# Performance work log

Hardware: AMD Instinct MI355X
Metric: run time of the kernel (lower is better)

The kernel has to match this reference:

```python
import jax, jax.numpy as jnp
import numpy as np


def setup_inputs() -> dict:
    key = jax.random.key(0)
    ks = jax.random.split(key, 6)
    B, C, H, W = 4, 512, 64, 64
    C8 = C // 8
    NS = H * W  # broadcasting in the original forces num_styles == H*W
    x = jax.random.normal(ks[0], (B, C, H, W), dtype=jnp.float32)
    Wq = jax.random.normal(ks[1], (C8, C), dtype=jnp.float32) * 0.02
    bq = jnp.zeros((C8,), jnp.float32)
    Wk = jax.random.normal(ks[2], (C8, C), dtype=jnp.float32) * 0.02
    bk = jnp.zeros((C8,), jnp.float32)
    Wv = jax.random.normal(ks[3], (C, C), dtype=jnp.float32) * 0.02
    bv = jnp.zeros((C,), jnp.float32)
    gamma = jnp.full((1,), 0.5, jnp.float32)  # nonzero so attention path contributes
    style_idx = jax.random.randint(ks[4], (B,), 0, NS)
    return {"x": x, "Wq": Wq, "bq": bq, "Wk": Wk, "bk": bk,
            "Wv": Wv, "bv": bv, "gamma": gamma,
            "style_idx": style_idx, "num_styles": NS}


def reference(x, Wq, bq, Wk, bk, Wv, bv, gamma, style_idx, num_styles):
    B, C, H, W = x.shape
    N = H * W
    xf = x.reshape(B, C, N)                                   # [B,C,N]
    # 1x1 convs == per-pixel linear projections
    q = jnp.einsum('oc,bcn->bno', Wq, xf) + bq                # [B,N,C8]
    k = jnp.einsum('oc,bcn->bon', Wk, xf) + bk[None, :, None]  # [B,C8,N]
    v = jnp.einsum('oc,bcn->bon', Wv, xf) + bv[None, :, None]  # [B,C,N]
    attn = jax.nn.softmax(jnp.einsum('bno,bom->bnm', q, k), axis=2)  # [B,N,N]
    # style mask: num_styles everywhere, except [b, 0, style_idx[b]] = 0
    # (torch scatter_ with index shape [B,1,1] only touches row 0)
    sw = jnp.full((B, N, num_styles), jnp.asarray(num_styles, x.dtype))
    sw = sw.at[jnp.arange(B), 0, style_idx].set(0.0)
    attn = attn * sw
    attended = jnp.einsum('bcn,bmn->bcm', v, attn).reshape(B, C, H, W)
    return gamma * attended + x
```

## Files before the change

kernel.cpp:

```cpp
#include <hip/hip_runtime.h>

#define B_DIM 4
#define C_DIM 512
#define N_DIM 4096
#define NS_F 4096.0f

typedef __attribute__((ext_vector_type(8))) short bf16x8;
typedef __attribute__((ext_vector_type(4))) float f32x4;

__device__ __forceinline__ unsigned short f2bf(float f) {
    union { float f; unsigned int u; } a; a.f = f;
    unsigned int u = a.u;
    return (unsigned short)((u + 0x7fffu + ((u >> 16) & 1u)) >> 16);
}
__device__ __forceinline__ float bf2f(unsigned short s) {
    union { unsigned int u; float f; } a; a.u = ((unsigned int)s) << 16;
    return a.f;
}

__global__ __launch_bounds__(256) void wconv_kernel(
    const float* __restrict__ Wq, const float* __restrict__ Wk,
    const float* __restrict__ Wv, unsigned short* __restrict__ Wb)
{
    const int gid = blockIdx.x * 256 + threadIdx.x;
    const int flat = gid * 4;
    const float* src;
    if (flat < 32768)      src = Wq + flat;
    else if (flat < 65536) src = Wk + (flat - 32768);
    else                   src = Wv + (flat - 65536);
    float4 v = *(const float4*)src;
    ushort4 r;
    r.x = f2bf(v.x); r.y = f2bf(v.y); r.z = f2bf(v.z); r.w = f2bf(v.w);
    *(ushort4*)(Wb + flat) = r;
}

__global__ __launch_bounds__(256) void xt_kernel(
    const float* __restrict__ x, unsigned short* __restrict__ xT)
{
    const int b  = blockIdx.z;
    const int c0 = blockIdx.y * 64;
    const int n0 = blockIdx.x * 64;
    __shared__ float T[64][65];
    const int t   = threadIdx.x;
    const int l16 = t & 15;
    const int cr  = t >> 4;

    #pragma unroll
    for (int j = 0; j < 4; ++j) {
        const int c = cr + j * 16;
        float4 v = *(const float4*)(x + ((size_t)(b * C_DIM + c0 + c)) * N_DIM + n0 + l16 * 4);
        T[l16 * 4 + 0][c] = v.x;
        T[l16 * 4 + 1][c] = v.y;
        T[l16 * 4 + 2][c] = v.z;
        T[l16 * 4 + 3][c] = v.w;
    }
    __syncthreads();
    #pragma unroll
    for (int j = 0; j < 2; ++j) {
        const int chunk = t + j * 256;
        const int n  = chunk >> 3;
        const int c8 = (chunk & 7) * 8;
        bf16x8 r;
        #pragma unroll
        for (int e = 0; e < 8; ++e) r[e] = (short)f2bf(T[n][c8 + e]);
        *(bf16x8*)(xT + ((size_t)b * N_DIM + n0 + n) * 512 + c0 + c8) = r;
    }
}

__global__ __launch_bounds__(256, 4) void proj_kernel(
    const unsigned short* __restrict__ xT, const unsigned short* __restrict__ Wb,
    const float* __restrict__ bq, const float* __restrict__ bk,
    const float* __restrict__ bv,
    unsigned short* __restrict__ qB, unsigned short* __restrict__ kB,
    unsigned short* __restrict__ vB)
{
    const int ot = blockIdx.x;
    const int n0 = blockIdx.y * 64;
    const int b  = blockIdx.z;
    const int tid  = threadIdx.x;
    const int w    = tid >> 6;
    const int lane = tid & 63;
    const int lql  = lane & 15;
    const int lk4  = lane >> 4;

    f32x4 acc[4];
    #pragma unroll
    for (int og = 0; og < 4; ++og) acc[og] = (f32x4){0.f, 0.f, 0.f, 0.f};

    if (ot < 2) {
        const unsigned short* Wp = Wb + ot * 32768;
        const unsigned short* xa = xT + ((size_t)b * N_DIM + n0 + w * 16 + lql) * 512 + lk4 * 8;
        for (int c0 = 0; c0 < 512; c0 += 32) {
            bf16x8 a = *(const bf16x8*)(xa + c0);
            #pragma unroll
            for (int og = 0; og < 4; ++og) {
                bf16x8 wf = *(const bf16x8*)(Wp + (size_t)(og * 16 + lql) * 512 + c0 + lk4 * 8);
                acc[og] = __builtin_amdgcn_mfma_f32_16x16x32_bf16(a, wf, acc[og], 0, 0, 0);
            }
        }
        const float* bias = (ot == 0) ? bq : bk;
        #pragma unroll
        for (int og = 0; og < 4; ++og) {
            const float bb = bias[og * 16 + lql];
            #pragma unroll
            for (int r = 0; r < 4; ++r) {
                const int n = n0 + w * 16 + lk4 * 4 + r;
                const unsigned short val = f2bf(acc[og][r] + bb);
                if (ot == 0) {
                    qB[((size_t)b * N_DIM + n) * 64 + og * 16 + lql] = val;
                } else {
                    const int o = og * 16 + lql;
                    kB[((size_t)b * N_DIM + n) * 64 + (o ^ ((n & 7) << 3))] = val;
                }
            }
        }
    } else {
        const int cb0 = (ot - 2) * 64;
        const unsigned short* wa = Wb + 65536 + (size_t)(cb0 + w * 16 + lql) * 512 + lk4 * 8;
        const unsigned short* xb = xT + (size_t)b * N_DIM * 512;
        for (int c0 = 0; c0 < 512; c0 += 32) {
            bf16x8 a = *(const bf16x8*)(wa + c0);
            #pragma unroll
            for (int og = 0; og < 4; ++og) {
                bf16x8 xf = *(const bf16x8*)(xb + (size_t)(n0 + og * 16 + lql) * 512 + c0 + lk4 * 8);
                acc[og] = __builtin_amdgcn_mfma_f32_16x16x32_bf16(a, xf, acc[og], 0, 0, 0);
            }
        }
        #pragma unroll
        for (int r = 0; r < 4; ++r) {
            const int c = cb0 + w * 16 + lk4 * 4 + r;
            const float bb = bv[c];
            #pragma unroll
            for (int og = 0; og < 4; ++og) {
                vB[((size_t)(b * C_DIM + c)) * N_DIM + n0 + og * 16 + lql] =
                    f2bf(acc[og][r] + bb);
            }
        }
    }
}

__global__ __launch_bounds__(256, 4) void flash_kernel(
    const unsigned short* __restrict__ qB,
    const unsigned short* __restrict__ kB,
    const unsigned short* __restrict__ vB,
    const float* __restrict__ x,
    const float* __restrict__ gamma,
    float* __restrict__ stats,
    float* __restrict__ out)
{
    const int bid   = blockIdx.x;
    const int low3  = bid & 7;
    const int b     = low3 >> 1;
    const int c0bit = low3 & 1;
    const int high  = bid >> 3;
    const int mt    = high >> 1;
    const int ch    = ((high & 1) << 1) | c0bit;
    const int m0    = mt * 64;

    const int tid  = threadIdx.x;
    const int w    = tid >> 6;
    const int lane = tid & 63;
    const int lql  = lane & 15;
    const int lk4  = lane >> 4;
    const int swz  = (lql & 7) << 3;

    __shared__ __align__(16) unsigned short Kl[2][4096];
    __shared__ __align__(16) unsigned short Pl[4096];
    __shared__ float scl[64];
    __shared__ float ll[64];
    __shared__ int   fl[4];

    const unsigned short* qrow = qB + ((size_t)b * N_DIM + m0 + w * 16 + lql) * 64 + lk4 * 8;
    const bf16x8 qf0 = *(const bf16x8*)(qrow);
    const bf16x8 qf1 = *(const bf16x8*)(qrow + 32);

    f32x4 acc[2][4];
    #pragma unroll
    for (int cg = 0; cg < 2; ++cg)
        #pragma unroll
        for (int qg = 0; qg < 4; ++qg)
            acc[cg][qg] = (f32x4){0.f, 0.f, 0.f, 0.f};

    float m_run = -3.0e38f;
    float l_run = 0.f;

    const unsigned short* kbb = kB + (size_t)b * N_DIM * 64;
    const unsigned short* vbb = vB + (size_t)b * C_DIM * N_DIM;
    const int cs = ch * 128 + w * 32;

    {
        bf16x8 a0 = *(const bf16x8*)(kbb + tid * 16);
        bf16x8 a1 = *(const bf16x8*)(kbb + tid * 16 + 8);
        *(bf16x8*)(&Kl[0][tid * 16]) = a0;
        *(bf16x8*)(&Kl[0][tid * 16 + 8]) = a1;
    }
    __syncthreads();

    int buf = 0;
    for (int t = 0; t < 64; ++t) {
        const int tn_ = (t + 1) & 63;
        const bf16x8 kn0 = *(const bf16x8*)(kbb + (size_t)tn_ * 4096 + tid * 16);
        const bf16x8 kn1 = *(const bf16x8*)(kbb + (size_t)tn_ * 4096 + tid * 16 + 8);

        f32x4 s[4];
        #pragma unroll
        for (int g = 0; g < 4; ++g) {
            const unsigned short* kr = &Kl[buf][(g * 16 + lql) * 64];
            bf16x8 ka0 = *(const bf16x8*)(kr + ((lk4 * 8) ^ swz));
            bf16x8 ka1 = *(const bf16x8*)(kr + ((lk4 * 8 + 32) ^ swz));
            f32x4 z = (f32x4){0.f, 0.f, 0.f, 0.f};
            z = __builtin_amdgcn_mfma_f32_16x16x32_bf16(ka0, qf0, z, 0, 0, 0);
            z = __builtin_amdgcn_mfma_f32_16x16x32_bf16(ka1, qf1, z, 0, 0, 0);
            s[g] = z;
        }

        float pmax = s[0][0];
        #pragma unroll
        for (int g = 0; g < 4; ++g)
            #pragma unroll
            for (int r = 0; r < 4; ++r)
                pmax = fmaxf(pmax, s[g][r]);
        pmax = fmaxf(pmax, __shfl_xor(pmax, 16));
        pmax = fmaxf(pmax, __shfl_xor(pmax, 32));

        const int wflag = __any(pmax > m_run + 8.f);
        float scv = 1.f;
        if (wflag) {
            const float nm = fmaxf(m_run, pmax);
            scv = __expf(m_run - nm);
            m_run = nm;
        }
        float p[4][4];
        float ps = 0.f;
        #pragma unroll
        for (int g = 0; g < 4; ++g)
            #pragma unroll
            for (int r = 0; r < 4; ++r) {
                p[g][r] = __expf(s[g][r] - m_run);
                ps += p[g][r];
            }
        ps += __shfl_xor(ps, 16);
        ps += __shfl_xor(ps, 32);
        l_run = l_run * scv + ps;

        if (lk4 == 0) scl[w * 16 + lql] = scv;
        if (lane == 0) fl[w] = wflag;

        {
            const int prow = (w * 16 + lql) * 64;
            #pragma unroll
            for (int g = 0; g < 4; ++g) {
                unsigned int lo = (unsigned int)f2bf(p[g][0]) | ((unsigned int)f2bf(p[g][1]) << 16);
                unsigned int hi = (unsigned int)f2bf(p[g][2]) | ((unsigned int)f2bf(p[g][3]) << 16);
                *(uint2*)(&Pl[prow + ((g * 16 + lk4 * 4) ^ swz)]) = make_uint2(lo, hi);
            }
        }
        __syncthreads();

        *(bf16x8*)(&Kl[buf ^ 1][tid * 16]) = kn0;
        *(bf16x8*)(&Kl[buf ^ 1][tid * 16 + 8]) = kn1;

        const int bflag = fl[0] | fl[1] | fl[2] | fl[3];
        if (bflag) {
            float sc4[4];
            #pragma unroll
            for (int qg = 0; qg < 4; ++qg) sc4[qg] = scl[qg * 16 + lql];
            #pragma unroll
            for (int cg = 0; cg < 2; ++cg)
                #pragma unroll
                for (int qg = 0; qg < 4; ++qg) {
                    acc[cg][qg][0] *= sc4[qg];
                    acc[cg][qg][1] *= sc4[qg];
                    acc[cg][qg][2] *= sc4[qg];
                    acc[cg][qg][3] *= sc4[qg];
                }
        }

        bf16x8 pf[4][2];
        #pragma unroll
        for (int qg = 0; qg < 4; ++qg) {
            const unsigned short* pr = &Pl[(qg * 16 + lql) * 64];
            pf[qg][0] = *(const bf16x8*)(pr + ((lk4 * 8) ^ swz));
            pf[qg][1] = *(const bf16x8*)(pr + ((lk4 * 8 + 32) ^ swz));
        }

        const int n0 = t * 64;
        const unsigned short* vpb = vbb + (size_t)(cs + lql) * N_DIM + n0 + lk4 * 8;
        __builtin_amdgcn_s_setprio(1);
        #pragma unroll
        for (int cg = 0; cg < 2; ++cg) {
            const unsigned short* vp = vpb + (size_t)cg * 16 * N_DIM;
            bf16x8 va0 = *(const bf16x8*)(vp);
            bf16x8 va1 = *(const bf16x8*)(vp + 32);
            #pragma unroll
            for (int qg = 0; qg < 4; ++qg) {
                acc[cg][qg] = __builtin_amdgcn_mfma_f32_16x16x32_bf16(va0, pf[qg][0], acc[cg][qg], 0, 0, 0);
                acc[cg][qg] = __builtin_amdgcn_mfma_f32_16x16x32_bf16(va1, pf[qg][1], acc[cg][qg], 0, 0, 0);
            }
        }
        __builtin_amdgcn_s_setprio(0);
        __syncthreads();
        buf ^= 1;
    }

    if (mt == 0 && ch == 0 && tid == 0) {
        stats[b * 2 + 0] = m_run;
        stats[b * 2 + 1] = l_run;
    }

    if (lk4 == 0) ll[w * 16 + lql] = l_run;
    __syncthreads();

    const float gns = gamma[0] * NS_F;
    float inv4[4];
    #pragma unroll
    for (int qg = 0; qg < 4; ++qg) inv4[qg] = 1.f / ll[qg * 16 + lql];

    #pragma unroll
    for (int cg = 0; cg < 2; ++cg) {
        #pragma unroll
        for (int r = 0; r < 4; ++r) {
            const int c = cs + cg * 16 + lk4 * 4 + r;
            const size_t rowb = ((size_t)b * C_DIM + c) * N_DIM;
            #pragma unroll
            for (int qg = 0; qg < 4; ++qg) {
                const int mg = m0 + qg * 16 + lql;
                out[rowb + mg] = fmaf(gns * inv4[qg], acc[cg][qg][r], x[rowb + mg]);
            }
        }
    }
}

__global__ __launch_bounds__(512) void patch_kernel(
    const unsigned short* __restrict__ qB,
    const unsigned short* __restrict__ kB,
    const unsigned short* __restrict__ vB,
    const float* __restrict__ stats,
    const float* __restrict__ gamma,
    const int* __restrict__ sidx,
    float* __restrict__ out)
{
    const int b = blockIdx.x;
    const int c = threadIdx.x;
    __shared__ float q0s[64];
    if (c < 64) q0s[c] = bf2f(qB[(size_t)b * N_DIM * 64 + c]);
    __syncthreads();
    const int s  = sidx[b];
    const int m7 = s & 7;
    const unsigned short* kr = kB + ((size_t)b * N_DIM + s) * 64;
    float logit = 0.f;
    #pragma unroll
    for (int dj = 0; dj < 8; ++dj) {
        const int slot = dj ^ m7;
        bf16x8 kv = *(const bf16x8*)(kr + slot * 8);
        #pragma unroll
        for (int e = 0; e < 8; ++e)
            logit = fmaf(bf2f((unsigned short)kv[e]), q0s[dj * 8 + e], logit);
    }
    const float corr = NS_F * __expf(logit - stats[b * 2]) / stats[b * 2 + 1];
    const float g = gamma[0];
    const float vcs = bf2f(vB[((size_t)b * C_DIM + c) * N_DIM + s]);
    out[((size_t)b * C_DIM + c) * N_DIM] -= g * corr * vcs;
}

extern "C" void kernel_launch(void* const* d_in, const int* in_sizes, int n_in,
                              void* d_out, int out_size, void* d_ws, size_t ws_size,
                              hipStream_t stream)
{
    const float* x     = (const float*)d_in[0];
    const float* Wq    = (const float*)d_in[1];
    const float* bq    = (const float*)d_in[2];
    const float* Wk    = (const float*)d_in[3];
    const float* bk    = (const float*)d_in[4];
    const float* Wv    = (const float*)d_in[5];
    const float* bv    = (const float*)d_in[6];
    const float* gamma = (const float*)d_in[7];
    const int*   sidx  = (const int*)d_in[8];
    float* out = (float*)d_out;

    unsigned short* xT = (unsigned short*)d_ws;
    unsigned short* Wb = xT + (size_t)B_DIM * N_DIM * 512;
    unsigned short* qB = Wb + 327680;
    unsigned short* kB = qB + (size_t)B_DIM * N_DIM * 64;
    unsigned short* vB = kB + (size_t)B_DIM * N_DIM * 64;
    float* stats = (float*)(vB + (size_t)B_DIM * C_DIM * N_DIM);

    wconv_kernel<<<dim3(320), 256, 0, stream>>>(Wq, Wk, Wv, Wb);
    xt_kernel<<<dim3(64, 8, B_DIM), 256, 0, stream>>>(x, xT);
    proj_kernel<<<dim3(10, 64, B_DIM), 256, 0, stream>>>(xT, Wb, bq, bk, bv, qB, kB, vB);
    flash_kernel<<<dim3(1024), 256, 0, stream>>>(qB, kB, vB, x, gamma, stats, out);
    patch_kernel<<<dim3(B_DIM), 512, 0, stream>>>(qB, kB, vB, stats, gamma, sidx, out);
}
```

Before: 350.7 us.

## Fold log2e into Q, use exp2, padded P tile, hw bf16 pack, unrolled projections

```diff
diff --git a/kernel.cpp b/kernel.cpp
--- a/kernel.cpp
+++ b/kernel.cpp
@@ -4,6 +4,7 @@
 #define C_DIM 512
 #define N_DIM 4096
 #define NS_F 4096.0f
+#define LOG2E_F 1.4426950408889634f
 
 typedef __attribute__((ext_vector_type(8))) short bf16x8;
 typedef __attribute__((ext_vector_type(4))) float f32x4;
@@ -67,7 +68,7 @@
     }
 }
 
-__global__ __launch_bounds__(256, 4) void proj_kernel(
+__global__ __launch_bounds__(256, 2) void proj_kernel(
     const unsigned short* __restrict__ xT, const unsigned short* __restrict__ Wb,
     const float* __restrict__ bq, const float* __restrict__ bk,
     const float* __restrict__ bv,
@@ -90,12 +91,19 @@
     if (ot < 2) {
         const unsigned short* Wp = Wb + ot * 32768;
         const unsigned short* xa = xT + ((size_t)b * N_DIM + n0 + w * 16 + lql) * 512 + lk4 * 8;
-        for (int c0 = 0; c0 < 512; c0 += 32) {
-            bf16x8 a = *(const bf16x8*)(xa + c0);
-            #pragma unroll
-            for (int og = 0; og < 4; ++og) {
-                bf16x8 wf = *(const bf16x8*)(Wp + (size_t)(og * 16 + lql) * 512 + c0 + lk4 * 8);
-                acc[og] = __builtin_amdgcn_mfma_f32_16x16x32_bf16(a, wf, acc[og], 0, 0, 0);
+        #pragma unroll
+        for (int h = 0; h < 2; ++h) {
+            bf16x8 af[8];
+            #pragma unroll
+            for (int i = 0; i < 8; ++i)
+                af[i] = *(const bf16x8*)(xa + (h * 8 + i) * 32);
+            #pragma unroll
+            for (int i = 0; i < 8; ++i) {
+                #pragma unroll
+                for (int og = 0; og < 4; ++og) {
+                    bf16x8 wf = *(const bf16x8*)(Wp + (size_t)(og * 16 + lql) * 512 + (h * 8 + i) * 32 + lk4 * 8);
+                    acc[og] = __builtin_amdgcn_mfma_f32_16x16x32_bf16(af[i], wf, acc[og], 0, 0, 0);
+                }
             }
         }
         const float* bias = (ot == 0) ? bq : bk;
@@ -105,12 +113,13 @@
             #pragma unroll
             for (int r = 0; r < 4; ++r) {
                 const int n = n0 + w * 16 + lk4 * 4 + r;
-                const unsigned short val = f2bf(acc[og][r] + bb);
                 if (ot == 0) {
-                    qB[((size_t)b * N_DIM + n) * 64 + og * 16 + lql] = val;
+                    qB[((size_t)b * N_DIM + n) * 64 + og * 16 + lql] =
+                        f2bf((acc[og][r] + bb) * LOG2E_F);
                 } else {
                     const int o = og * 16 + lql;
-                    kB[((size_t)b * N_DIM + n) * 64 + (o ^ ((n & 7) << 3))] = val;
+                    kB[((size_t)b * N_DIM + n) * 64 + (o ^ ((n & 7) << 3))] =
+                        f2bf(acc[og][r] + bb);
                 }
             }
         }
@@ -118,12 +127,19 @@
         const int cb0 = (ot - 2) * 64;
         const unsigned short* wa = Wb + 65536 + (size_t)(cb0 + w * 16 + lql) * 512 + lk4 * 8;
         const unsigned short* xb = xT + (size_t)b * N_DIM * 512;
-        for (int c0 = 0; c0 < 512; c0 += 32) {
-            bf16x8 a = *(const bf16x8*)(wa + c0);
-            #pragma unroll
-            for (int og = 0; og < 4; ++og) {
-                bf16x8 xf = *(const bf16x8*)(xb + (size_t)(n0 + og * 16 + lql) * 512 + c0 + lk4 * 8);
-                acc[og] = __builtin_amdgcn_mfma_f32_16x16x32_bf16(a, xf, acc[og], 0, 0, 0);
+        #pragma unroll
+        for (int h = 0; h < 2; ++h) {
+            bf16x8 af[8];
+            #pragma unroll
+            for (int i = 0; i < 8; ++i)
+                af[i] = *(const bf16x8*)(wa + (h * 8 + i) * 32);
+            #pragma unroll
+            for (int i = 0; i < 8; ++i) {
+                #pragma unroll
+                for (int og = 0; og < 4; ++og) {
+                    bf16x8 xf = *(const bf16x8*)(xb + (size_t)(n0 + og * 16 + lql) * 512 + (h * 8 + i) * 32 + lk4 * 8);
+                    acc[og] = __builtin_amdgcn_mfma_f32_16x16x32_bf16(af[i], xf, acc[og], 0, 0, 0);
+                }
             }
         }
         #pragma unroll
@@ -165,7 +181,7 @@
     const int swz  = (lql & 7) << 3;
 
     __shared__ __align__(16) unsigned short Kl[2][4096];
-    __shared__ __align__(16) unsigned short Pl[4096];
+    __shared__ __align__(16) unsigned short Pl[64][72];
     __shared__ float scl[64];
     __shared__ float ll[64];
     __shared__ int   fl[4];
@@ -189,18 +205,18 @@
     const int cs = ch * 128 + w * 32;
 
     {
-        bf16x8 a0 = *(const bf16x8*)(kbb + tid * 16);
-        bf16x8 a1 = *(const bf16x8*)(kbb + tid * 16 + 8);
-        *(bf16x8*)(&Kl[0][tid * 16]) = a0;
-        *(bf16x8*)(&Kl[0][tid * 16 + 8]) = a1;
+        bf16x8 a0 = *(const bf16x8*)(kbb + tid * 8);
+        bf16x8 a1 = *(const bf16x8*)(kbb + 2048 + tid * 8);
+        *(bf16x8*)(&Kl[0][tid * 8]) = a0;
+        *(bf16x8*)(&Kl[0][2048 + tid * 8]) = a1;
     }
     __syncthreads();
 
     int buf = 0;
     for (int t = 0; t < 64; ++t) {
         const int tn_ = (t + 1) & 63;
-        const bf16x8 kn0 = *(const bf16x8*)(kbb + (size_t)tn_ * 4096 + tid * 16);
-        const bf16x8 kn1 = *(const bf16x8*)(kbb + (size_t)tn_ * 4096 + tid * 16 + 8);
+        const bf16x8 kn0 = *(const bf16x8*)(kbb + (size_t)tn_ * 4096 + tid * 8);
+        const bf16x8 kn1 = *(const bf16x8*)(kbb + (size_t)tn_ * 4096 + 2048 + tid * 8);
 
         f32x4 s[4];
         #pragma unroll
@@ -227,7 +243,7 @@
         float scv = 1.f;
         if (wflag) {
             const float nm = fmaxf(m_run, pmax);
-            scv = __expf(m_run - nm);
+            scv = exp2f(m_run - nm);
             m_run = nm;
         }
         float p[4][4];
@@ -236,7 +252,7 @@
         for (int g = 0; g < 4; ++g)
             #pragma unroll
             for (int r = 0; r < 4; ++r) {
-                p[g][r] = __expf(s[g][r] - m_run);
+                p[g][r] = exp2f(s[g][r] - m_run);
                 ps += p[g][r];
             }
         ps += __shfl_xor(ps, 16);
@@ -247,18 +263,19 @@
         if (lane == 0) fl[w] = wflag;
 
         {
-            const int prow = (w * 16 + lql) * 64;
+            unsigned short* prow = &Pl[w * 16 + lql][0];
             #pragma unroll
             for (int g = 0; g < 4; ++g) {
-                unsigned int lo = (unsigned int)f2bf(p[g][0]) | ((unsigned int)f2bf(p[g][1]) << 16);
-                unsigned int hi = (unsigned int)f2bf(p[g][2]) | ((unsigned int)f2bf(p[g][3]) << 16);
-                *(uint2*)(&Pl[prow + ((g * 16 + lk4 * 4) ^ swz)]) = make_uint2(lo, hi);
+                unsigned int lo, hi;
+                asm("v_cvt_pk_bf16_f32 %0, %1, %2" : "=v"(lo) : "v"(p[g][0]), "v"(p[g][1]));
+                asm("v_cvt_pk_bf16_f32 %0, %1, %2" : "=v"(hi) : "v"(p[g][2]), "v"(p[g][3]));
+                *(uint2*)(prow + g * 16 + lk4 * 4) = make_uint2(lo, hi);
             }
         }
         __syncthreads();
 
-        *(bf16x8*)(&Kl[buf ^ 1][tid * 16]) = kn0;
-        *(bf16x8*)(&Kl[buf ^ 1][tid * 16 + 8]) = kn1;
+        *(bf16x8*)(&Kl[buf ^ 1][tid * 8]) = kn0;
+        *(bf16x8*)(&Kl[buf ^ 1][2048 + tid * 8]) = kn1;
 
         const int bflag = fl[0] | fl[1] | fl[2] | fl[3];
         if (bflag) {
@@ -279,9 +296,9 @@
         bf16x8 pf[4][2];
         #pragma unroll
         for (int qg = 0; qg < 4; ++qg) {
-            const unsigned short* pr = &Pl[(qg * 16 + lql) * 64];
-            pf[qg][0] = *(const bf16x8*)(pr + ((lk4 * 8) ^ swz));
-            pf[qg][1] = *(const bf16x8*)(pr + ((lk4 * 8 + 32) ^ swz));
+            const unsigned short* pr = &Pl[qg * 16 + lql][0];
+            pf[qg][0] = *(const bf16x8*)(pr + lk4 * 8);
+            pf[qg][1] = *(const bf16x8*)(pr + lk4 * 8 + 32);
         }
 
         const int n0 = t * 64;
@@ -357,7 +374,7 @@
         for (int e = 0; e < 8; ++e)
             logit = fmaf(bf2f((unsigned short)kv[e]), q0s[dj * 8 + e], logit);
     }
-    const float corr = NS_F * __expf(logit - stats[b * 2]) / stats[b * 2 + 1];
+    const float corr = NS_F * exp2f(logit - stats[b * 2]) / stats[b * 2 + 1];
     const float g = gamma[0];
     const float vcs = bf2f(vB[((size_t)b * C_DIM + c) * N_DIM + s]);
     out[((size_t)b * C_DIM + c) * N_DIM] -= g * corr * vcs;
```

Result: slower. 366.7 us (+4.6%).
